# Performance work log

Measured on AMD Instinct MI355X. Metric: run time of the kernel, lower is better.

Reference implementation:

```python
import jax, jax.numpy as jnp
import numpy as np

B, S, D, L = 32, 1024, 768, 12

def setup_inputs() -> dict:
    key = jax.random.key(0)
    ks = jax.random.split(key, 10)
    hidden_states = jax.random.normal(ks[0], (B, S, D), dtype=jnp.float32)
    Wq = jax.random.normal(ks[1], (L, D, D), dtype=jnp.float32) * 0.02
    Wk = jax.random.normal(ks[2], (L, D, D), dtype=jnp.float32) * 0.02
    Wv = jax.random.normal(ks[3], (L, D, D), dtype=jnp.float32) * 0.02
    bq = jnp.zeros((L, D), dtype=jnp.float32)
    bk = jnp.zeros((L, D), dtype=jnp.float32)
    bv = jnp.zeros((L, D), dtype=jnp.float32)
    l_k = jnp.full((L, D), 0.8, dtype=jnp.float32)  # iA3 scales, init 0.8 per source
    l_v = jnp.full((L, D), 0.8, dtype=jnp.float32)
    W_head = jax.random.normal(ks[4], (D, 1), dtype=jnp.float32) * 0.02
    b_head = jnp.zeros((1,), dtype=jnp.float32)
    return {"hidden_states": hidden_states, "Wq": Wq, "bq": bq, "Wk": Wk, "bk": bk,
            "Wv": Wv, "bv": bv, "l_k": l_k, "l_v": l_v, "W_head": W_head, "b_head": b_head}

def reference(hidden_states, Wq, bq, Wk, bk, Wv, bv, l_k, l_v, W_head, b_head):
    scale = 1.0 / jnp.sqrt(jnp.float32(D))

    def layer_step(h, params):
        wq, bq_i, wk, bk_i, wv, bv_i, lk, lv = params
        Q = jnp.einsum('bsd,de->bse', h, wq) + bq_i
        K = (jnp.einsum('bsd,de->bse', h, wk) + bk_i) * lk  # iA3 per-channel scale on K
        V = (jnp.einsum('bsd,de->bse', h, wv) + bv_i) * lv  # iA3 per-channel scale on V
        attn = jax.nn.softmax(jnp.einsum('bqd,bkd->bqk', Q, K) * scale, axis=-1)
        h_new = jnp.einsum('bqk,bkd->bqd', attn, V)  # note: no residual/LN, matches source
        return h_new, None

    h, _ = jax.lax.scan(layer_step, hidden_states, (Wq, bq, Wk, bk, Wv, bv, l_k, l_v))
    pooled = h[:, 0, :]  # CLS token
    out = pooled @ W_head + b_head  # [B, 1]
    return out[:, 0]
```

## Files before the change

kernel.cpp:

```cpp
#include <hip/hip_runtime.h>
#include <hip/hip_fp16.h>
#include <math.h>

#define B_ 32
#define S_ 1024
#define D_ 768
#define L_ 12
#define SD 786432LL
#define SS 1048576LL
#define DD 589824LL
#define LDL 1769472LL

typedef _Float16 half8 __attribute__((ext_vector_type(8)));
typedef float f32x4 __attribute__((ext_vector_type(4)));
typedef unsigned short u16;

#define SW(lr) ((((lr) ^ ((lr) >> 3)) & 7))

#define GLD16(p, o) __builtin_amdgcn_global_load_lds( \
        (const __attribute__((address_space(1))) void*)(p), \
        (__attribute__((address_space(3))) void*)&smem[o], 16, 0, 0)


__global__ __launch_bounds__(256, 3)
void gemm_qkv_k(const __half* __restrict__ A, const __half* __restrict__ Wt,
                const float* __restrict__ biasC, const float* __restrict__ scaleC,
                float aBias,
                __half* __restrict__ CQ, __half* __restrict__ CK, __half* __restrict__ CVt,
                int nBase, int tilesX, int mPerXcd)
{
    __shared__ __align__(16) u16 smem[24576];
    const int K = 768;

    const int flat = blockIdx.x;
    const int xcd = flat & 7;
    const int jj = flat >> 3;
    const int mLocal = jj / tilesX;
    const int nxI = jj - mLocal * tilesX;
    const int n0 = nxI * 128;
    const int m0 = (xcd * mPerXcd + mLocal) * 128;

    const int t = threadIdx.x;
    const int l = t & 63, w = t >> 6;
    const int wm = (w & 1) * 64, wn = (w >> 1) * 64;

    const int u0 = t, u1 = t + 256;
    const int r0 = u0 >> 2, c0 = (u0 & 3) ^ ((r0 >> 1) & 3);
    const int r1 = u1 >> 2, c1 = (u1 & 3) ^ ((r1 >> 1) & 3);
    const __half* gA0 = A + (long long)(m0 + r0) * K + c0 * 8;
    const __half* gA1 = A + (long long)(m0 + r1) * K + c1 * 8;
    const __half* gB0 = Wt + (long long)(n0 + r0) * K + c0 * 8;
    const __half* gB1 = Wt + (long long)(n0 + r1) * K + c1 * 8;

    int aoff[4], boff[4];
    const int kc = l >> 4;
    #pragma unroll
    for (int mt = 0; mt < 4; ++mt) {
        int rr = wm + mt * 16 + (l & 15);
        aoff[mt] = (rr * 4 + (kc ^ ((rr >> 1) & 3))) * 8;
        int rb = wn + mt * 16 + (l & 15);
        boff[mt] = (rb * 4 + (kc ^ ((rb >> 1) & 3))) * 8;
    }

    f32x4 acc[4][4];
    #pragma unroll
    for (int i = 0; i < 4; ++i)
        #pragma unroll
        for (int j = 0; j < 4; ++j)
            acc[i][j] = (f32x4){0.f, 0.f, 0.f, 0.f};

    GLD16(gA0,      u0 * 8);                 GLD16(gA1,      u1 * 8);
    GLD16(gB0,      12288 + u0 * 8);         GLD16(gB1,      12288 + u1 * 8);
    GLD16(gA0 + 32, 4096 + u0 * 8);          GLD16(gA1 + 32, 4096 + u1 * 8);
    GLD16(gB0 + 32, 12288 + 4096 + u0 * 8);  GLD16(gB1 + 32, 12288 + 4096 + u1 * 8);

    int cur = 0;
    #pragma unroll 3
    for (int k0 = 0; k0 < K; k0 += 32) {
        if (k0 + 32 < K) asm volatile("s_waitcnt vmcnt(4)\n\ts_barrier" ::: "memory");
        else             asm volatile("s_waitcnt vmcnt(0)\n\ts_barrier" ::: "memory");
        if (k0 + 64 < K) {
            const int ts = (cur + 2 >= 3) ? (cur - 1) : (cur + 2);
            const int tsa = ts * 4096, tsb = 12288 + ts * 4096;
            GLD16(gA0 + k0 + 64, tsa + u0 * 8);  GLD16(gA1 + k0 + 64, tsa + u1 * 8);
            GLD16(gB0 + k0 + 64, tsb + u0 * 8);  GLD16(gB1 + k0 + 64, tsb + u1 * 8);
        }
        const int sa = cur * 4096, sb = 12288 + cur * 4096;
        half8 af[4], bf[4];
        #pragma unroll
        for (int mt = 0; mt < 4; ++mt) af[mt] = *(const half8*)(const void*)&smem[sa + aoff[mt]];
        #pragma unroll
        for (int nt = 0; nt < 4; ++nt) bf[nt] = *(const half8*)(const void*)&smem[sb + boff[nt]];
        #pragma unroll
        for (int nt = 0; nt < 4; ++nt)
            #pragma unroll
            for (int mt = 0; mt < 4; ++mt)
                acc[mt][nt] = __builtin_amdgcn_mfma_f32_16x16x32_f16(af[mt], bf[nt], acc[mt][nt], 0, 0, 0);
        __builtin_amdgcn_sched_barrier(0);
        cur = (cur >= 2) ? 0 : (cur + 1);
    }
    __syncthreads();

    const int nCat0 = n0 + nBase;
    const int region = nCat0 / 768;
    const int colBase = nCat0 - region * 768;

    float badd[4], bmul[4];
    #pragma unroll
    for (int nt = 0; nt < 4; ++nt) {
        int gn = nCat0 + wn + nt * 16 + (l & 15);
        badd[nt] = aBias * biasC[gn];
        bmul[nt] = scaleC[gn];
    }

    const int qbase = w * 4096;
    #pragma unroll
    for (int mt = 0; mt < 4; ++mt) {
        #pragma unroll
        for (int nt = 0; nt < 4; ++nt) {
            #pragma unroll
            for (int i = 0; i < 4; ++i) {
                int lrow = mt * 16 + ((l >> 4) << 2) + i;
                int lcol = nt * 16 + (l & 15);
                float v = (acc[mt][nt][i] + badd[nt]) * bmul[nt];
                int cc = lcol >> 3, c7 = lcol & 7;
                smem[qbase + lrow * 64 + ((cc ^ SW(lrow)) << 3) + c7] =
                    __half_as_ushort(__float2half(v));
            }
        }
    }
    __syncthreads();

    if (region < 2) {
        __half* Creg = region ? CK : CQ;
        #pragma unroll
        for (int p = 0; p < 8; ++p) {
            int u = t + p * 256;
            int R = u >> 4, cc = u & 15;
            int qb = ((R >> 6) + ((cc >> 3) << 1)) * 4096;
            int lr = R & 63, lcc = cc & 7;
            half8 val = *(const half8*)(const void*)&smem[qb + lr * 64 + ((lcc ^ SW(lr)) << 3)];
            *(half8*)(void*)&Creg[(long long)(m0 + R) * 768 + colBase + cc * 8] = val;
        }
    } else {
        #pragma unroll
        for (int p = 0; p < 8; ++p) {
            int u = t + p * 256;
            int Crow = u >> 4, mcc = u & 15;
            __align__(16) u16 tmp[8];
            #pragma unroll
            for (int j = 0; j < 8; ++j) {
                int m = mcc * 8 + j;
                int qb = ((m >> 6) + ((Crow >> 6) << 1)) * 4096;
                int lr = m & 63, lcol = Crow & 63;
                int lcc = lcol >> 3;
                tmp[j] = smem[qb + lr * 64 + ((lcc ^ SW(lr)) << 3) + (lcol & 7)];
            }
            long long b = m0 >> 10;
            __half* dst = CVt + b * SD + (long long)(colBase + Crow) * 1024 + (m0 & 1023) + mcc * 8;
            *(half8*)(void*)dst = *(const half8*)(const void*)tmp;
        }
    }
}

template<int SWIZ, int MODE>
__global__ __launch_bounds__(256, 3)
void gemm_att_k(const __half* __restrict__ A, const __half* __restrict__ B,
                float aAcc, __half* __restrict__ C, int K, int ldc,
                long long sA, long long sB, long long sC,
                int tilesX, int tilesPB, int bpx,
                float* __restrict__ rsp, const float* __restrict__ invsum)
{
    __shared__ __align__(16) u16 smem[24576];
    float* sums = (float*)(void*)&smem[16384];

    int nxI, ny;
    long long bz;
    if (SWIZ) {
        int flat = blockIdx.x;
        int xcd = flat & 7;
        int j = flat >> 3;
        int bLocal = j / tilesPB;
        int tt = j - bLocal * tilesPB;
        bz = (long long)(xcd * bpx + bLocal);
        ny = tt / tilesX;
        nxI = tt - ny * tilesX;
    } else {
        nxI = blockIdx.x; ny = blockIdx.y; bz = blockIdx.z;
    }

    const int t = threadIdx.x;
    const int l = t & 63, w = t >> 6;
    const int n0 = nxI * 128;
    const int m0 = ny * 128;
    A += bz * sA; B += bz * sB; C += bz * sC;

    const int wm = (w & 1) * 64, wn = (w >> 1) * 64;

    const int u0 = t, u1 = t + 256;
    const int r0 = u0 >> 2, c0 = (u0 & 3) ^ ((r0 >> 1) & 3);
    const int r1 = u1 >> 2, c1 = (u1 & 3) ^ ((r1 >> 1) & 3);
    const __half* gA0 = A + (long long)(m0 + r0) * K + c0 * 8;
    const __half* gA1 = A + (long long)(m0 + r1) * K + c1 * 8;
    const __half* gB0 = B + (long long)(n0 + r0) * K + c0 * 8;
    const __half* gB1 = B + (long long)(n0 + r1) * K + c1 * 8;

    int aoff[4], boff[4];
    const int kc = l >> 4;
    #pragma unroll
    for (int mt = 0; mt < 4; ++mt) {
        int rr = wm + mt * 16 + (l & 15);
        aoff[mt] = (rr * 4 + (kc ^ ((rr >> 1) & 3))) * 8;
        int rb = wn + mt * 16 + (l & 15);
        boff[mt] = (rb * 4 + (kc ^ ((rb >> 1) & 3))) * 8;
    }

    f32x4 acc[4][4];
    #pragma unroll
    for (int i = 0; i < 4; ++i)
        #pragma unroll
        for (int j = 0; j < 4; ++j)
            acc[i][j] = (f32x4){0.f, 0.f, 0.f, 0.f};

    GLD16(gA0,      u0 * 8);                 GLD16(gA1,      u1 * 8);
    GLD16(gB0,      12288 + u0 * 8);         GLD16(gB1,      12288 + u1 * 8);
    GLD16(gA0 + 32, 4096 + u0 * 8);          GLD16(gA1 + 32, 4096 + u1 * 8);
    GLD16(gB0 + 32, 12288 + 4096 + u0 * 8);  GLD16(gB1 + 32, 12288 + 4096 + u1 * 8);

    int cur = 0;
    #pragma unroll 3
    for (int k0 = 0; k0 < K; k0 += 32) {
        if (k0 + 32 < K) asm volatile("s_waitcnt vmcnt(4)\n\ts_barrier" ::: "memory");
        else             asm volatile("s_waitcnt vmcnt(0)\n\ts_barrier" ::: "memory");
        if (k0 + 64 < K) {
            const int ts = (cur + 2 >= 3) ? (cur - 1) : (cur + 2);
            const int tsa = ts * 4096, tsb = 12288 + ts * 4096;
            GLD16(gA0 + k0 + 64, tsa + u0 * 8);  GLD16(gA1 + k0 + 64, tsa + u1 * 8);
            GLD16(gB0 + k0 + 64, tsb + u0 * 8);  GLD16(gB1 + k0 + 64, tsb + u1 * 8);
        }
        const int sa = cur * 4096, sb = 12288 + cur * 4096;
        half8 af[4], bf[4];
        #pragma unroll
        for (int mt = 0; mt < 4; ++mt) af[mt] = *(const half8*)(const void*)&smem[sa + aoff[mt]];
        #pragma unroll
        for (int nt = 0; nt < 4; ++nt) bf[nt] = *(const half8*)(const void*)&smem[sb + boff[nt]];
        #pragma unroll
        for (int nt = 0; nt < 4; ++nt)
            #pragma unroll
            for (int mt = 0; mt < 4; ++mt)
                acc[mt][nt] = __builtin_amdgcn_mfma_f32_16x16x32_f16(af[mt], bf[nt], acc[mt][nt], 0, 0, 0);
        __builtin_amdgcn_sched_barrier(0);
        cur = (cur >= 2) ? 0 : (cur + 1);
    }
    __syncthreads();

    float invr[4][4];
    if (MODE == 2) {
        #pragma unroll
        for (int mt = 0; mt < 4; ++mt)
            #pragma unroll
            for (int i = 0; i < 4; ++i)
                invr[mt][i] = invsum[bz * 1024 + m0 + wm + mt * 16 + ((l >> 4) << 2) + i];
    }

    const int qbase = w * 4096;
    #pragma unroll
    for (int mt = 0; mt < 4; ++mt) {
        #pragma unroll
        for (int nt = 0; nt < 4; ++nt) {
            #pragma unroll
            for (int i = 0; i < 4; ++i) {
                int lrow = mt * 16 + ((l >> 4) << 2) + i;
                int lcol = nt * 16 + (l & 15);
                float v;
                if (MODE == 1)      v = __expf(acc[mt][nt][i] * aAcc);
                else                v = acc[mt][nt][i] * aAcc * invr[mt][i];
                int cc = lcol >> 3, c7 = lcol & 7;
                smem[qbase + lrow * 64 + ((cc ^ SW(lrow)) << 3) + c7] =
                    __half_as_ushort(__float2half(v));
            }
        }
    }
    __syncthreads();

    #pragma unroll
    for (int p = 0; p < 8; ++p) {
        int u = t + p * 256;
        int R = u >> 4, cc = u & 15;
        int qb = ((R >> 6) + ((cc >> 3) << 1)) * 4096;
        int lr = R & 63, lcc = cc & 7;
        half8 val = *(const half8*)(const void*)&smem[qb + lr * 64 + ((lcc ^ SW(lr)) << 3)];
        *(half8*)(void*)&C[(long long)(m0 + R) * ldc + n0 + cc * 8] = val;
        if (MODE == 1) {
            float s8 = 0.f;
            #pragma unroll
            for (int j = 0; j < 8; ++j) s8 += (float)val[j];
            sums[R * 17 + cc] = s8;
        }
    }
    if (MODE == 1) {
        __syncthreads();
        if (t < 128) {
            float s = 0.f;
            #pragma unroll
            for (int c = 0; c < 16; ++c) s += sums[t * 17 + c];
            rsp[bz * 8192 + (long long)(m0 + t) * 8 + nxI] = s;
        }
    }
}

__global__ __launch_bounds__(256)
void rowsuminv_k(const float* __restrict__ rsp, float* __restrict__ inv, int n)
{
    int i = blockIdx.x * 256 + threadIdx.x;
    if (i < n) {
        const float* p = rsp + (long long)i * 8;
        float s = ((p[0] + p[1]) + (p[2] + p[3])) + ((p[4] + p[5]) + (p[6] + p[7]));
        inv[i] = 1.0f / s;
    }
}

__global__ __launch_bounds__(256)
void cvt32to16_k(const float* __restrict__ X, __half* __restrict__ Y)
{
    long long i = ((long long)blockIdx.x * 256 + threadIdx.x) * 4;
    float4 v = *(const float4*)&X[i];
    *(__half2*)&Y[i]     = __floats2half2_rn(v.x, v.y);
    *(__half2*)&Y[i + 2] = __floats2half2_rn(v.z, v.w);
}

__global__ __launch_bounds__(256)
void wtrans_k(const float* __restrict__ W, __half* __restrict__ Wt,
              long long ldL, int rowOff)
{
    __shared__ float Ls[64][65];
    const int lyr = blockIdx.z;
    const int k0 = blockIdx.y * 64, n0 = blockIdx.x * 64;
    const float* src = W + (long long)lyr * DD;
    __half* dst = Wt + (long long)lyr * ldL;
    const int t = threadIdx.x;
    #pragma unroll
    for (int p = 0; p < 4; ++p) {
        int u = t + p * 256;
        int r = u >> 4, c4 = (u & 15) * 4;
        float4 v = *(const float4*)&src[(long long)(k0 + r) * D_ + n0 + c4];
        Ls[r][c4] = v.x; Ls[r][c4 + 1] = v.y; Ls[r][c4 + 2] = v.z; Ls[r][c4 + 3] = v.w;
    }
    __syncthreads();
    #pragma unroll
    for (int p = 0; p < 2; ++p) {
        int u = t + p * 256;
        int n = u >> 3, kc8 = (u & 7) * 8;
        __align__(16) u16 tmp[8];
        #pragma unroll
        for (int j = 0; j < 8; ++j) {
            _Float16 h = (_Float16)Ls[kc8 + j][n];
            tmp[j] = *(const u16*)&h;
        }
        *(half8*)(void*)&dst[(long long)(rowOff + n0 + n) * D_ + k0 + kc8] =
            *(const half8*)(const void*)tmp;
    }
}

__global__ __launch_bounds__(256)
void bscat_k(const float* __restrict__ bq, const float* __restrict__ bk,
             const float* __restrict__ bv, const float* __restrict__ lk,
             const float* __restrict__ lv, float* __restrict__ bsb,
             float* __restrict__ bss)
{
    int i = blockIdx.x * 256 + threadIdx.x;
    if (i >= L_ * 2304) return;
    int l = i / 2304, p = i - l * 2304;
    int r = p / 768, c = p - r * 768;
    float b, s;
    if (r == 0)      { b = bq[l * 768 + c]; s = 1.f; }
    else if (r == 1) { b = bk[l * 768 + c]; s = lk[l * 768 + c]; }
    else             { b = bv[l * 768 + c]; s = lv[l * 768 + c]; }
    bsb[i] = b; bss[i] = s;
}

__global__ __launch_bounds__(256)
void q0_k(const __half* __restrict__ H16, const __half* __restrict__ Wcat,
          const float* __restrict__ bq, float* __restrict__ q0f, float sig)
{
    const int b = blockIdx.x;
    const int n = blockIdx.y * 256 + threadIdx.x;
    const int t = threadIdx.x;
    __shared__ __half hrow[768];
    const __half* h = H16 + (long long)b * SD;
    hrow[t] = h[t]; hrow[t + 256] = h[t + 256]; hrow[t + 512] = h[t + 512];
    __syncthreads();
    const __half* wr = Wcat + 11LL * LDL + (long long)n * 768;
    float acc = 0.f;
    for (int k = 0; k < 768; ++k) acc += (float)hrow[k] * (float)wr[k];
    q0f[b * 768 + n] = acc + sig * bq[11 * 768 + n];
}

__global__ __launch_bounds__(256)
void s0_k(const float* __restrict__ q0f, const __half* __restrict__ K16,
          float* __restrict__ s0f, int b0, float aQK)
{
    const int z = blockIdx.x;
    const int b = b0 + z;
    const int s = blockIdx.y * 256 + threadIdx.x;
    const int t = threadIdx.x;
    __shared__ float qrow[768];
    qrow[t] = q0f[b * 768 + t];
    qrow[t + 256] = q0f[b * 768 + t + 256];
    qrow[t + 512] = q0f[b * 768 + t + 512];
    __syncthreads();
    const __half* kr = K16 + (long long)z * SD + (long long)s * 768;
    float acc = 0.f;
    for (int k = 0; k < 768; ++k) acc += qrow[k] * (float)kr[k];
    s0f[b * 1024 + s] = acc * aQK;
}

__global__ __launch_bounds__(256)
void sm0_k(float* __restrict__ s0f, int b0)
{
    float* p = s0f + (long long)(b0 + blockIdx.x) * 1024;
    const int t = threadIdx.x;
    float v[4];
    float mx = -1e30f;
    #pragma unroll
    for (int j = 0; j < 4; ++j) { v[j] = p[t + 256 * j]; mx = fmaxf(mx, v[j]); }
    __shared__ float red[256];
    red[t] = mx; __syncthreads();
    for (int s = 128; s > 0; s >>= 1) { if (t < s) red[t] = fmaxf(red[t], red[t + s]); __syncthreads(); }
    mx = red[0];
    __syncthreads();
    float sum = 0.f;
    #pragma unroll
    for (int j = 0; j < 4; ++j) { v[j] = __expf(v[j] - mx); sum += v[j]; }
    red[t] = sum; __syncthreads();
    for (int s = 128; s > 0; s >>= 1) { if (t < s) red[t] += red[t + s]; __syncthreads(); }
    const float inv = 1.0f / red[0];
    __syncthreads();
    #pragma unroll
    for (int j = 0; j < 4; ++j) p[t + 256 * j] = v[j] * inv;
}

__global__ __launch_bounds__(256)
void o0_k(const float* __restrict__ p0f, const __half* __restrict__ Vt16,
          float* __restrict__ o0f, int b0, float invSig)
{
    const int z = blockIdx.x;
    const int b = b0 + z;
    const int d = blockIdx.y * 256 + threadIdx.x;
    const int t = threadIdx.x;
    __shared__ float prow[1024];
    #pragma unroll
    for (int j = 0; j < 4; ++j) prow[t + 256 * j] = p0f[b * 1024 + t + 256 * j];
    __syncthreads();
    const __half* vr = Vt16 + (long long)z * SD + (long long)d * 1024;
    float acc = 0.f;
    for (int s = 0; s < 1024; ++s) acc += prow[s] * (float)vr[s];
    o0f[b * 768 + d] = acc * invSig;
}

__global__ __launch_bounds__(256)
void headf_k(const float* __restrict__ o0f, const float* __restrict__ Wh,
             const float* __restrict__ bh, float* __restrict__ out)
{
    const int b = blockIdx.x;
    const int t = threadIdx.x;
    float s = 0.f;
    for (int d = t; d < 768; d += 256) s += o0f[b * 768 + d] * Wh[d];
    __shared__ float red[256];
    red[t] = s; __syncthreads();
    for (int k = 128; k > 0; k >>= 1) { if (t < k) red[t] += red[t + k]; __syncthreads(); }
    if (t == 0) out[b] = red[0] + bh[0];
}

extern "C" void kernel_launch(void* const* d_in, const int* in_sizes, int n_in,
                              void* d_out, int out_size, void* d_ws, size_t ws_size,
                              hipStream_t stream)
{
    const float* hs = (const float*)d_in[0];
    const float* Wq = (const float*)d_in[1];
    const float* bq = (const float*)d_in[2];
    const float* Wk = (const float*)d_in[3];
    const float* bk = (const float*)d_in[4];
    const float* Wv = (const float*)d_in[5];
    const float* bv = (const float*)d_in[6];
    const float* lk = (const float*)d_in[7];
    const float* lv = (const float*)d_in[8];
    const float* Wh = (const float*)d_in[9];
    const float* bh = (const float*)d_in[10];
    float* outp = (float*)d_out;

    __half* H16  = (__half*)d_ws;
    __half* Wcat = H16 + (long long)B_ * SD;
    float*  bsb  = (float*)(Wcat + 12LL * LDL);
    float*  bss  = bsb + 12 * 2304;
    float*  q0f  = bss + 12 * 2304;
    float*  s0f  = q0f + 32 * 768;
    float*  o0f  = s0f + 32 * 1024;
    float*  rsp  = o0f + 32 * 768;
    float*  inv  = rsp + 32LL * 8192;
    __half* Q16  = (__half*)(inv + 32 * 1024);

    const size_t baseBytes = (size_t)((char*)Q16 - (char*)d_ws);
    const size_t perG = ((size_t)(3 * SD) + (size_t)SS) * 2;
    long long avail = (long long)ws_size - (long long)baseBytes;
    int G = (avail > 0) ? (int)(avail / perG) : 1;
    if (G >= 32) G = 32; else if (G >= 16) G = 16; else if (G >= 8) G = 8;
    if (G < 1) G = 1;
    __half* K16  = Q16 + (long long)G * SD;
    __half* Vt16 = K16 + (long long)G * SD;
    __half* P16  = Vt16 + (long long)G * SD;

    cvt32to16_k<<<dim3((int)((B_ * SD) / 1024)), 256, 0, stream>>>(hs, H16);
    wtrans_k<<<dim3(12, 12, 12), 256, 0, stream>>>(Wq, Wcat, LDL, 0);
    wtrans_k<<<dim3(12, 12, 12), 256, 0, stream>>>(Wk, Wcat, LDL, 768);
    wtrans_k<<<dim3(12, 12, 12), 256, 0, stream>>>(Wv, Wcat, LDL, 1536);
    bscat_k<<<dim3((L_ * 2304 + 255) / 256), 256, 0, stream>>>(bq, bk, bv, lk, lv, bsb, bss);

    const float scq = 0.036084391824351615f;
    float sig = 1.f;

    for (int lyr = 0; lyr < L_ - 1; ++lyr) {
        const __half* W = Wcat + (long long)lyr * LDL;
        const float* bb = bsb + lyr * 2304;
        const float* ss = bss + lyr * 2304;
        const float aQK = scq / (sig * sig);

        for (int b0 = 0; b0 < B_; b0 += G) {
            const int nb = (B_ - b0 < G) ? (B_ - b0) : G;
            const __half* hg = H16 + (long long)b0 * SD;

            gemm_qkv_k<<<dim3(18 * 8 * nb), 256, 0, stream>>>(
                hg, W, bb, ss, sig, Q16, K16, Vt16, 0, 18, nb);

            if ((nb & 7) == 0) {
                gemm_att_k<1, 1><<<dim3(nb * 64), 256, 0, stream>>>(
                    Q16, K16, aQK, P16, 768, 1024, SD, SD, SS, 8, 64, nb >> 3, rsp, nullptr);
            } else {
                gemm_att_k<0, 1><<<dim3(8, 8, nb), 256, 0, stream>>>(
                    Q16, K16, aQK, P16, 768, 1024, SD, SD, SS, 8, 64, 1, rsp, nullptr);
            }

            rowsuminv_k<<<dim3(nb * 4), 256, 0, stream>>>(rsp, inv, nb * 1024);

            if ((nb & 7) == 0) {
                gemm_att_k<1, 2><<<dim3(nb * 48), 256, 0, stream>>>(
                    P16, Vt16, 4.f, H16 + (long long)b0 * SD, 1024, 768, SS, SD, SD,
                    6, 48, nb >> 3, nullptr, inv);
            } else {
                gemm_att_k<0, 2><<<dim3(6, 8, nb), 256, 0, stream>>>(
                    P16, Vt16, 4.f, H16 + (long long)b0 * SD, 1024, 768, SS, SD, SD,
                    6, 48, 1, nullptr, inv);
            }
        }
        sig *= 4.f;
    }

    const float aQK = scq / (sig * sig);
    q0_k<<<dim3(B_, 3), 256, 0, stream>>>(H16, Wcat, bq, q0f, sig);

    for (int b0 = 0; b0 < B_; b0 += G) {
        const int nb = (B_ - b0 < G) ? (B_ - b0) : G;
        const __half* hg = H16 + (long long)b0 * SD;

        gemm_qkv_k<<<dim3(12 * 8 * nb), 256, 0, stream>>>(
            hg, Wcat + 11LL * LDL + 768LL * 768, bsb + 11 * 2304, bss + 11 * 2304,
            sig, K16 , K16, Vt16, 768, 12, nb);

        s0_k<<<dim3(nb, 4), 256, 0, stream>>>(q0f, K16, s0f, b0, aQK);
        sm0_k<<<dim3(nb), 256, 0, stream>>>(s0f, b0);
        o0_k<<<dim3(nb, 3), 256, 0, stream>>>(s0f, Vt16, o0f, b0, 1.f / sig);
    }

    headf_k<<<dim3(B_), 256, 0, stream>>>(o0f, Wh, bh, outp);
}
```

Measured before the change: 3.482 ms.

## Enlarge QKV and QK^T GEMM tiles to 256x128 with 8x4 MFMA per wave

The QKV projection and the QK^T score GEMM now use 256x128 output tiles: each wave computes 128x64 with 32 accumulators, and shared memory grows to 72KB with occupancy lowered to 2 blocks. The QK^T kernel is split from the PV kernel and computes row-sum partials with wave shuffles instead of a second LDS pass and barrier. The epilogue LDS layout becomes a single 128-column swizzled tile. Larger tiles raise arithmetic intensity per byte loaded, at the cost of fewer resident waves, higher register pressure and fewer blocks to fill the GPU.

```diff
diff --git a/kernel.cpp b/kernel.cpp
--- a/kernel.cpp
+++ b/kernel.cpp
@@ -22,80 +22,96 @@
         (__attribute__((address_space(3))) void*)&smem[o], 16, 0, 0)
 
 
-__global__ __launch_bounds__(256, 3)
+template<int SWIZ>
+__global__ __launch_bounds__(256, 2)
 void gemm_qkv_k(const __half* __restrict__ A, const __half* __restrict__ Wt,
                 const float* __restrict__ biasC, const float* __restrict__ scaleC,
                 float aBias,
                 __half* __restrict__ CQ, __half* __restrict__ CK, __half* __restrict__ CVt,
                 int nBase, int tilesX, int mPerXcd)
 {
-    __shared__ __align__(16) u16 smem[24576];
+    __shared__ __align__(16) u16 smem[36864];
     const int K = 768;
 
-    const int flat = blockIdx.x;
-    const int xcd = flat & 7;
-    const int jj = flat >> 3;
-    const int mLocal = jj / tilesX;
-    const int nxI = jj - mLocal * tilesX;
+    int mIdx, nxI;
+    if (SWIZ) {
+        const int flat = blockIdx.x;
+        const int xcd = flat & 7;
+        const int jj = flat >> 3;
+        const int mLocal = jj / tilesX;
+        nxI = jj - mLocal * tilesX;
+        mIdx = xcd * mPerXcd + mLocal;
+    } else {
+        mIdx = blockIdx.x / tilesX;
+        nxI = blockIdx.x - mIdx * tilesX;
+    }
+    const int m0 = mIdx * 256;
     const int n0 = nxI * 128;
-    const int m0 = (xcd * mPerXcd + mLocal) * 128;
 
     const int t = threadIdx.x;
     const int l = t & 63, w = t >> 6;
-    const int wm = (w & 1) * 64, wn = (w >> 1) * 64;
-
-    const int u0 = t, u1 = t + 256;
-    const int r0 = u0 >> 2, c0 = (u0 & 3) ^ ((r0 >> 1) & 3);
-    const int r1 = u1 >> 2, c1 = (u1 & 3) ^ ((r1 >> 1) & 3);
-    const __half* gA0 = A + (long long)(m0 + r0) * K + c0 * 8;
-    const __half* gA1 = A + (long long)(m0 + r1) * K + c1 * 8;
-    const __half* gB0 = Wt + (long long)(n0 + r0) * K + c0 * 8;
-    const __half* gB1 = Wt + (long long)(n0 + r1) * K + c1 * 8;
-
-    int aoff[4], boff[4];
-    const int kc = l >> 4;
-    #pragma unroll
-    for (int mt = 0; mt < 4; ++mt) {
-        int rr = wm + mt * 16 + (l & 15);
-        aoff[mt] = (rr * 4 + (kc ^ ((rr >> 1) & 3))) * 8;
-        int rb = wn + mt * 16 + (l & 15);
-        boff[mt] = (rb * 4 + (kc ^ ((rb >> 1) & 3))) * 8;
-    }
-
-    f32x4 acc[4][4];
-    #pragma unroll
-    for (int i = 0; i < 4; ++i)
+    const int wm = (w & 1) * 128, wn = (w >> 1) * 64;
+    const int q = l >> 4, lr = l & 15;
+
+    const int uA0 = t, uA1 = t + 256, uA2 = t + 512, uA3 = t + 768;
+    const int uB0 = t, uB1 = t + 256;
+#define MKA(u) (A + (long long)(m0 + ((u) >> 2)) * K + ((((u) & 3) ^ ((((u) >> 2) >> 1) & 3)) * 8))
+#define MKB(u) (Wt + (long long)(n0 + ((u) >> 2)) * K + ((((u) & 3) ^ ((((u) >> 2) >> 1) & 3)) * 8))
+    const __half* gA0 = MKA(uA0); const __half* gA1 = MKA(uA1);
+    const __half* gA2 = MKA(uA2); const __half* gA3 = MKA(uA3);
+    const __half* gB0 = MKB(uB0); const __half* gB1 = MKB(uB1);
+#undef MKA
+#undef MKB
+
+    int aoff[8], boff[4];
+    #pragma unroll
+    for (int mf = 0; mf < 8; ++mf) {
+        int rr = wm + mf * 16 + lr;
+        aoff[mf] = (rr * 4 + (q ^ ((rr >> 1) & 3))) * 8;
+    }
+    #pragma unroll
+    for (int nf = 0; nf < 4; ++nf) {
+        int rb = wn + nf * 16 + lr;
+        boff[nf] = (rb * 4 + (q ^ ((rb >> 1) & 3))) * 8;
+    }
+
+    f32x4 acc[8][4];
+    #pragma unroll
+    for (int i = 0; i < 8; ++i)
         #pragma unroll
         for (int j = 0; j < 4; ++j)
             acc[i][j] = (f32x4){0.f, 0.f, 0.f, 0.f};
 
-    GLD16(gA0,      u0 * 8);                 GLD16(gA1,      u1 * 8);
-    GLD16(gB0,      12288 + u0 * 8);         GLD16(gB1,      12288 + u1 * 8);
-    GLD16(gA0 + 32, 4096 + u0 * 8);          GLD16(gA1 + 32, 4096 + u1 * 8);
-    GLD16(gB0 + 32, 12288 + 4096 + u0 * 8);  GLD16(gB1 + 32, 12288 + 4096 + u1 * 8);
+    GLD16(gA0, uA0 * 8); GLD16(gA1, uA1 * 8); GLD16(gA2, uA2 * 8); GLD16(gA3, uA3 * 8);
+    GLD16(gB0, 8192 + uB0 * 8); GLD16(gB1, 8192 + uB1 * 8);
+    GLD16(gA0 + 32, 12288 + uA0 * 8); GLD16(gA1 + 32, 12288 + uA1 * 8);
+    GLD16(gA2 + 32, 12288 + uA2 * 8); GLD16(gA3 + 32, 12288 + uA3 * 8);
+    GLD16(gB0 + 32, 12288 + 8192 + uB0 * 8); GLD16(gB1 + 32, 12288 + 8192 + uB1 * 8);
 
     int cur = 0;
     #pragma unroll 3
     for (int k0 = 0; k0 < K; k0 += 32) {
-        if (k0 + 32 < K) asm volatile("s_waitcnt vmcnt(4)\n\ts_barrier" ::: "memory");
+        if (k0 + 32 < K) asm volatile("s_waitcnt vmcnt(6)\n\ts_barrier" ::: "memory");
         else             asm volatile("s_waitcnt vmcnt(0)\n\ts_barrier" ::: "memory");
         if (k0 + 64 < K) {
             const int ts = (cur + 2 >= 3) ? (cur - 1) : (cur + 2);
-            const int tsa = ts * 4096, tsb = 12288 + ts * 4096;
-            GLD16(gA0 + k0 + 64, tsa + u0 * 8);  GLD16(gA1 + k0 + 64, tsa + u1 * 8);
-            GLD16(gB0 + k0 + 64, tsb + u0 * 8);  GLD16(gB1 + k0 + 64, tsb + u1 * 8);
-        }
-        const int sa = cur * 4096, sb = 12288 + cur * 4096;
-        half8 af[4], bf[4];
-        #pragma unroll
-        for (int mt = 0; mt < 4; ++mt) af[mt] = *(const half8*)(const void*)&smem[sa + aoff[mt]];
-        #pragma unroll
-        for (int nt = 0; nt < 4; ++nt) bf[nt] = *(const half8*)(const void*)&smem[sb + boff[nt]];
-        #pragma unroll
-        for (int nt = 0; nt < 4; ++nt)
+            const int tb = ts * 12288;
+            GLD16(gA0 + k0 + 64, tb + uA0 * 8); GLD16(gA1 + k0 + 64, tb + uA1 * 8);
+            GLD16(gA2 + k0 + 64, tb + uA2 * 8); GLD16(gA3 + k0 + 64, tb + uA3 * 8);
+            GLD16(gB0 + k0 + 64, tb + 8192 + uB0 * 8);
+            GLD16(gB1 + k0 + 64, tb + 8192 + uB1 * 8);
+        }
+        const int sa = cur * 12288, sb = sa + 8192;
+        half8 af[8], bf[4];
+        #pragma unroll
+        for (int mf = 0; mf < 8; ++mf) af[mf] = *(const half8*)(const void*)&smem[sa + aoff[mf]];
+        #pragma unroll
+        for (int nf = 0; nf < 4; ++nf) bf[nf] = *(const half8*)(const void*)&smem[sb + boff[nf]];
+        #pragma unroll
+        for (int nf = 0; nf < 4; ++nf)
             #pragma unroll
-            for (int mt = 0; mt < 4; ++mt)
-                acc[mt][nt] = __builtin_amdgcn_mfma_f32_16x16x32_f16(af[mt], bf[nt], acc[mt][nt], 0, 0, 0);
+            for (int mf = 0; mf < 8; ++mf)
+                acc[mf][nf] = __builtin_amdgcn_mfma_f32_16x16x32_f16(af[mf], bf[nf], acc[mf][nf], 0, 0, 0);
         __builtin_amdgcn_sched_barrier(0);
         cur = (cur >= 2) ? 0 : (cur + 1);
     }
@@ -108,23 +124,22 @@
     float badd[4], bmul[4];
     #pragma unroll
     for (int nt = 0; nt < 4; ++nt) {
-        int gn = nCat0 + wn + nt * 16 + (l & 15);
+        int gn = nCat0 + wn + nt * 16 + lr;
         badd[nt] = aBias * biasC[gn];
         bmul[nt] = scaleC[gn];
     }
 
-    const int qbase = w * 4096;
-    #pragma unroll
-    for (int mt = 0; mt < 4; ++mt) {
+    #pragma unroll
+    for (int mf = 0; mf < 8; ++mf) {
         #pragma unroll
         for (int nt = 0; nt < 4; ++nt) {
             #pragma unroll
             for (int i = 0; i < 4; ++i) {
-                int lrow = mt * 16 + ((l >> 4) << 2) + i;
-                int lcol = nt * 16 + (l & 15);
-                float v = (acc[mt][nt][i] + badd[nt]) * bmul[nt];
+                int lrow = wm + mf * 16 + q * 4 + i;
+                int lcol = wn + nt * 16 + lr;
+                float v = (acc[mf][nt][i] + badd[nt]) * bmul[nt];
                 int cc = lcol >> 3, c7 = lcol & 7;
-                smem[qbase + lrow * 64 + ((cc ^ SW(lrow)) << 3) + c7] =
+                smem[lrow * 128 + ((cc ^ (lrow & 15)) << 3) + c7] =
                     __half_as_ushort(__float2half(v));
             }
         }
@@ -134,45 +149,39 @@
     if (region < 2) {
         __half* Creg = region ? CK : CQ;
         #pragma unroll
-        for (int p = 0; p < 8; ++p) {
+        for (int p = 0; p < 16; ++p) {
             int u = t + p * 256;
             int R = u >> 4, cc = u & 15;
-            int qb = ((R >> 6) + ((cc >> 3) << 1)) * 4096;
-            int lr = R & 63, lcc = cc & 7;
-            half8 val = *(const half8*)(const void*)&smem[qb + lr * 64 + ((lcc ^ SW(lr)) << 3)];
+            half8 val = *(const half8*)(const void*)&smem[R * 128 + ((cc ^ (R & 15)) << 3)];
             *(half8*)(void*)&Creg[(long long)(m0 + R) * 768 + colBase + cc * 8] = val;
         }
     } else {
-        #pragma unroll
-        for (int p = 0; p < 8; ++p) {
+        long long b = m0 >> 10;
+        const int mrow0 = m0 & 1023;
+        #pragma unroll
+        for (int p = 0; p < 16; ++p) {
             int u = t + p * 256;
-            int Crow = u >> 4, mcc = u & 15;
+            int n = u >> 5, mc = u & 31;
             __align__(16) u16 tmp[8];
             #pragma unroll
             for (int j = 0; j < 8; ++j) {
-                int m = mcc * 8 + j;
-                int qb = ((m >> 6) + ((Crow >> 6) << 1)) * 4096;
-                int lr = m & 63, lcol = Crow & 63;
-                int lcc = lcol >> 3;
-                tmp[j] = smem[qb + lr * 64 + ((lcc ^ SW(lr)) << 3) + (lcol & 7)];
+                int m = mc * 8 + j;
+                tmp[j] = smem[m * 128 + ((((n >> 3) ^ (m & 15))) << 3) + (n & 7)];
             }
-            long long b = m0 >> 10;
-            __half* dst = CVt + b * SD + (long long)(colBase + Crow) * 1024 + (m0 & 1023) + mcc * 8;
+            __half* dst = CVt + b * SD + (long long)(colBase + n) * 1024 + mrow0 + mc * 8;
             *(half8*)(void*)dst = *(const half8*)(const void*)tmp;
         }
     }
 }
 
-template<int SWIZ, int MODE>
-__global__ __launch_bounds__(256, 3)
-void gemm_att_k(const __half* __restrict__ A, const __half* __restrict__ B,
-                float aAcc, __half* __restrict__ C, int K, int ldc,
-                long long sA, long long sB, long long sC,
-                int tilesX, int tilesPB, int bpx,
-                float* __restrict__ rsp, const float* __restrict__ invsum)
-{
-    __shared__ __align__(16) u16 smem[24576];
-    float* sums = (float*)(void*)&smem[16384];
+template<int SWIZ>
+__global__ __launch_bounds__(256, 2)
+void gemm_qk_k(const __half* __restrict__ A, const __half* __restrict__ B,
+               float aAcc, __half* __restrict__ C, float* __restrict__ rsp,
+               int tilesX, int tilesPB, int bpx)
+{
+    __shared__ __align__(16) u16 smem[36864];
+    const int K = 768;
 
     int nxI, ny;
     long long bz;
@@ -191,6 +200,139 @@
 
     const int t = threadIdx.x;
     const int l = t & 63, w = t >> 6;
+    const int m0 = ny * 256;
+    const int n0 = nxI * 128;
+    A += bz * SD; B += bz * SD; C += bz * SS;
+
+    const int wm = (w & 1) * 128, wn = (w >> 1) * 64;
+    const int q = l >> 4, lr = l & 15;
+
+    const int uA0 = t, uA1 = t + 256, uA2 = t + 512, uA3 = t + 768;
+    const int uB0 = t, uB1 = t + 256;
+#define MKA(u) (A + (long long)(m0 + ((u) >> 2)) * K + ((((u) & 3) ^ ((((u) >> 2) >> 1) & 3)) * 8))
+#define MKB(u) (B + (long long)(n0 + ((u) >> 2)) * K + ((((u) & 3) ^ ((((u) >> 2) >> 1) & 3)) * 8))
+    const __half* gA0 = MKA(uA0); const __half* gA1 = MKA(uA1);
+    const __half* gA2 = MKA(uA2); const __half* gA3 = MKA(uA3);
+    const __half* gB0 = MKB(uB0); const __half* gB1 = MKB(uB1);
+#undef MKA
+#undef MKB
+
+    int aoff[8], boff[4];
+    #pragma unroll
+    for (int mf = 0; mf < 8; ++mf) {
+        int rr = wm + mf * 16 + lr;
+        aoff[mf] = (rr * 4 + (q ^ ((rr >> 1) & 3))) * 8;
+    }
+    #pragma unroll
+    for (int nf = 0; nf < 4; ++nf) {
+        int rb = wn + nf * 16 + lr;
+        boff[nf] = (rb * 4 + (q ^ ((rb >> 1) & 3))) * 8;
+    }
+
+    f32x4 acc[8][4];
+    #pragma unroll
+    for (int i = 0; i < 8; ++i)
+        #pragma unroll
+        for (int j = 0; j < 4; ++j)
+            acc[i][j] = (f32x4){0.f, 0.f, 0.f, 0.f};
+
+    GLD16(gA0, uA0 * 8); GLD16(gA1, uA1 * 8); GLD16(gA2, uA2 * 8); GLD16(gA3, uA3 * 8);
+    GLD16(gB0, 8192 + uB0 * 8); GLD16(gB1, 8192 + uB1 * 8);
+    GLD16(gA0 + 32, 12288 + uA0 * 8); GLD16(gA1 + 32, 12288 + uA1 * 8);
+    GLD16(gA2 + 32, 12288 + uA2 * 8); GLD16(gA3 + 32, 12288 + uA3 * 8);
+    GLD16(gB0 + 32, 12288 + 8192 + uB0 * 8); GLD16(gB1 + 32, 12288 + 8192 + uB1 * 8);
+
+    int cur = 0;
+    #pragma unroll 3
+    for (int k0 = 0; k0 < K; k0 += 32) {
+        if (k0 + 32 < K) asm volatile("s_waitcnt vmcnt(6)\n\ts_barrier" ::: "memory");
+        else             asm volatile("s_waitcnt vmcnt(0)\n\ts_barrier" ::: "memory");
+        if (k0 + 64 < K) {
+            const int ts = (cur + 2 >= 3) ? (cur - 1) : (cur + 2);
+            const int tb = ts * 12288;
+            GLD16(gA0 + k0 + 64, tb + uA0 * 8); GLD16(gA1 + k0 + 64, tb + uA1 * 8);
+            GLD16(gA2 + k0 + 64, tb + uA2 * 8); GLD16(gA3 + k0 + 64, tb + uA3 * 8);
+            GLD16(gB0 + k0 + 64, tb + 8192 + uB0 * 8);
+            GLD16(gB1 + k0 + 64, tb + 8192 + uB1 * 8);
+        }
+        const int sa = cur * 12288, sb = sa + 8192;
+        half8 af[8], bf[4];
+        #pragma unroll
+        for (int mf = 0; mf < 8; ++mf) af[mf] = *(const half8*)(const void*)&smem[sa + aoff[mf]];
+        #pragma unroll
+        for (int nf = 0; nf < 4; ++nf) bf[nf] = *(const half8*)(const void*)&smem[sb + boff[nf]];
+        #pragma unroll
+        for (int nf = 0; nf < 4; ++nf)
+            #pragma unroll
+            for (int mf = 0; mf < 8; ++mf)
+                acc[mf][nf] = __builtin_amdgcn_mfma_f32_16x16x32_f16(af[mf], bf[nf], acc[mf][nf], 0, 0, 0);
+        __builtin_amdgcn_sched_barrier(0);
+        cur = (cur >= 2) ? 0 : (cur + 1);
+    }
+    __syncthreads();
+
+    #pragma unroll
+    for (int mf = 0; mf < 8; ++mf) {
+        #pragma unroll
+        for (int nt = 0; nt < 4; ++nt) {
+            #pragma unroll
+            for (int i = 0; i < 4; ++i) {
+                int lrow = wm + mf * 16 + q * 4 + i;
+                int lcol = wn + nt * 16 + lr;
+                float v = __expf(acc[mf][nt][i] * aAcc);
+                int cc = lcol >> 3, c7 = lcol & 7;
+                smem[lrow * 128 + ((cc ^ (lrow & 15)) << 3) + c7] =
+                    __half_as_ushort(__float2half(v));
+            }
+        }
+    }
+    __syncthreads();
+
+    #pragma unroll
+    for (int p = 0; p < 16; ++p) {
+        int u = t + p * 256;
+        int R = u >> 4, cc = u & 15;
+        half8 val = *(const half8*)(const void*)&smem[R * 128 + ((cc ^ (R & 15)) << 3)];
+        *(half8*)(void*)&C[(long long)(m0 + R) * 1024 + n0 + cc * 8] = val;
+        float s8 = 0.f;
+        #pragma unroll
+        for (int j = 0; j < 8; ++j) s8 += (float)val[j];
+        s8 += __shfl_xor(s8, 1, 16);
+        s8 += __shfl_xor(s8, 2, 16);
+        s8 += __shfl_xor(s8, 4, 16);
+        s8 += __shfl_xor(s8, 8, 16);
+        if ((l & 15) == 0)
+            rsp[bz * 8192 + (long long)(m0 + R) * 8 + nxI] = s8;
+    }
+}
+
+template<int SWIZ>
+__global__ __launch_bounds__(256, 3)
+void gemm_pv_k(const __half* __restrict__ A, const __half* __restrict__ B,
+               float aAcc, __half* __restrict__ C, int K, int ldc,
+               long long sA, long long sB, long long sC,
+               int tilesX, int tilesPB, int bpx,
+               const float* __restrict__ invsum)
+{
+    __shared__ __align__(16) u16 smem[24576];
+
+    int nxI, ny;
+    long long bz;
+    if (SWIZ) {
+        int flat = blockIdx.x;
+        int xcd = flat & 7;
+        int j = flat >> 3;
+        int bLocal = j / tilesPB;
+        int tt = j - bLocal * tilesPB;
+        bz = (long long)(xcd * bpx + bLocal);
+        ny = tt / tilesX;
+        nxI = tt - ny * tilesX;
+    } else {
+        nxI = blockIdx.x; ny = blockIdx.y; bz = blockIdx.z;
+    }
+
+    const int t = threadIdx.x;
+    const int l = t & 63, w = t >> 6;
     const int n0 = nxI * 128;
     const int m0 = ny * 128;
     A += bz * sA; B += bz * sB; C += bz * sC;
@@ -255,13 +397,11 @@
     __syncthreads();
 
     float invr[4][4];
-    if (MODE == 2) {
-        #pragma unroll
-        for (int mt = 0; mt < 4; ++mt)
-            #pragma unroll
-            for (int i = 0; i < 4; ++i)
-                invr[mt][i] = invsum[bz * 1024 + m0 + wm + mt * 16 + ((l >> 4) << 2) + i];
-    }
+    #pragma unroll
+    for (int mt = 0; mt < 4; ++mt)
+        #pragma unroll
+        for (int i = 0; i < 4; ++i)
+            invr[mt][i] = invsum[bz * 1024 + m0 + wm + mt * 16 + ((l >> 4) << 2) + i];
 
     const int qbase = w * 4096;
     #pragma unroll
@@ -272,9 +412,7 @@
             for (int i = 0; i < 4; ++i) {
                 int lrow = mt * 16 + ((l >> 4) << 2) + i;
                 int lcol = nt * 16 + (l & 15);
-                float v;
-                if (MODE == 1)      v = __expf(acc[mt][nt][i] * aAcc);
-                else                v = acc[mt][nt][i] * aAcc * invr[mt][i];
+                float v = acc[mt][nt][i] * aAcc * invr[mt][i];
                 int cc = lcol >> 3, c7 = lcol & 7;
                 smem[qbase + lrow * 64 + ((cc ^ SW(lrow)) << 3) + c7] =
                     __half_as_ushort(__float2half(v));
@@ -288,24 +426,9 @@
         int u = t + p * 256;
         int R = u >> 4, cc = u & 15;
         int qb = ((R >> 6) + ((cc >> 3) << 1)) * 4096;
-        int lr = R & 63, lcc = cc & 7;
-        half8 val = *(const half8*)(const void*)&smem[qb + lr * 64 + ((lcc ^ SW(lr)) << 3)];
+        int lr2 = R & 63, lcc = cc & 7;
+        half8 val = *(const half8*)(const void*)&smem[qb + lr2 * 64 + ((lcc ^ SW(lr2)) << 3)];
         *(half8*)(void*)&C[(long long)(m0 + R) * ldc + n0 + cc * 8] = val;
-        if (MODE == 1) {
-            float s8 = 0.f;
-            #pragma unroll
-            for (int j = 0; j < 8; ++j) s8 += (float)val[j];
-            sums[R * 17 + cc] = s8;
-        }
-    }
-    if (MODE == 1) {
-        __syncthreads();
-        if (t < 128) {
-            float s = 0.f;
-            #pragma unroll
-            for (int c = 0; c < 16; ++c) s += sums[t * 17 + c];
-            rsp[bz * 8192 + (long long)(m0 + t) * 8 + nxI] = s;
-        }
     }
 }
 
@@ -529,27 +652,32 @@
             const int nb = (B_ - b0 < G) ? (B_ - b0) : G;
             const __half* hg = H16 + (long long)b0 * SD;
 
-            gemm_qkv_k<<<dim3(18 * 8 * nb), 256, 0, stream>>>(
-                hg, W, bb, ss, sig, Q16, K16, Vt16, 0, 18, nb);
+            if ((nb & 1) == 0) {
+                gemm_qkv_k<1><<<dim3(8 * (nb >> 1) * 18), 256, 0, stream>>>(
+                    hg, W, bb, ss, sig, Q16, K16, Vt16, 0, 18, nb >> 1);
+            } else {
+                gemm_qkv_k<0><<<dim3(nb * 4 * 18), 256, 0, stream>>>(
+                    hg, W, bb, ss, sig, Q16, K16, Vt16, 0, 18, 0);
+            }
 
             if ((nb & 7) == 0) {
-                gemm_att_k<1, 1><<<dim3(nb * 64), 256, 0, stream>>>(
-                    Q16, K16, aQK, P16, 768, 1024, SD, SD, SS, 8, 64, nb >> 3, rsp, nullptr);
+                gemm_qk_k<1><<<dim3(nb * 32), 256, 0, stream>>>(
+                    Q16, K16, aQK, P16, rsp, 8, 32, nb >> 3);
             } else {
-                gemm_att_k<0, 1><<<dim3(8, 8, nb), 256, 0, stream>>>(
-                    Q16, K16, aQK, P16, 768, 1024, SD, SD, SS, 8, 64, 1, rsp, nullptr);
+                gemm_qk_k<0><<<dim3(8, 4, nb), 256, 0, stream>>>(
+                    Q16, K16, aQK, P16, rsp, 8, 32, 1);
             }
 
             rowsuminv_k<<<dim3(nb * 4), 256, 0, stream>>>(rsp, inv, nb * 1024);
 
             if ((nb & 7) == 0) {
-                gemm_att_k<1, 2><<<dim3(nb * 48), 256, 0, stream>>>(
+                gemm_pv_k<1><<<dim3(nb * 48), 256, 0, stream>>>(
                     P16, Vt16, 4.f, H16 + (long long)b0 * SD, 1024, 768, SS, SD, SD,
-                    6, 48, nb >> 3, nullptr, inv);
+                    6, 48, nb >> 3, inv);
             } else {
-                gemm_att_k<0, 2><<<dim3(6, 8, nb), 256, 0, stream>>>(
+                gemm_pv_k<0><<<dim3(6, 8, nb), 256, 0, stream>>>(
                     P16, Vt16, 4.f, H16 + (long long)b0 * SD, 1024, 768, SS, SD, SD,
-                    6, 48, 1, nullptr, inv);
+                    6, 48, 1, inv);
             }
         }
         sig *= 4.f;
@@ -562,9 +690,15 @@
         const int nb = (B_ - b0 < G) ? (B_ - b0) : G;
         const __half* hg = H16 + (long long)b0 * SD;
 
-        gemm_qkv_k<<<dim3(12 * 8 * nb), 256, 0, stream>>>(
-            hg, Wcat + 11LL * LDL + 768LL * 768, bsb + 11 * 2304, bss + 11 * 2304,
-            sig, K16 , K16, Vt16, 768, 12, nb);
+        if ((nb & 1) == 0) {
+            gemm_qkv_k<1><<<dim3(8 * (nb >> 1) * 12), 256, 0, stream>>>(
+                hg, Wcat + 11LL * LDL + 768LL * 768, bsb + 11 * 2304, bss + 11 * 2304,
+                sig, K16 , K16, Vt16, 768, 12, nb >> 1);
+        } else {
+            gemm_qkv_k<0><<<dim3(nb * 4 * 12), 256, 0, stream>>>(
+                hg, Wcat + 11LL * LDL + 768LL * 768, bsb + 11 * 2304, bss + 11 * 2304,
+                sig, K16 , K16, Vt16, 768, 12, 0);
+        }
 
         s0_k<<<dim3(nb, 4), 256, 0, stream>>>(q0f, K16, s0f, b0, aQK);
         sm0_k<<<dim3(nb), 256, 0, stream>>>(s0f, b0);
```

Result: slower. 3.796 ms (+9.0%).

## Enlarge QKV GEMM tile to 256x128 with per-wave 128x64 sub-tiles

Applied to the files above, without the earlier changes.

The QKV projection GEMM now computes 256x128 output tiles instead of 128x128, with each wave holding a 128x64 accumulator block (8x4 MFMA fragments). This doubles A-side reuse of each B fragment and halves the number of blocks. Shared memory grows to 72 KB, launch bounds drop to 2 blocks per CU, and the epilogue is rewritten with a 128-wide swizzled staging layout. A non-XCD-swizzled variant covers odd batch-group counts. The cost is higher register pressure and fewer resident waves.

```diff
diff --git a/kernel.cpp b/kernel.cpp
--- a/kernel.cpp
+++ b/kernel.cpp
@@ -16,86 +16,102 @@
 typedef unsigned short u16;
 
 #define SW(lr) ((((lr) ^ ((lr) >> 3)) & 7))
+#define KEY16(r) (((r) ^ ((r) >> 3)) & 15)
 
 #define GLD16(p, o) __builtin_amdgcn_global_load_lds( \
         (const __attribute__((address_space(1))) void*)(p), \
         (__attribute__((address_space(3))) void*)&smem[o], 16, 0, 0)
 
-
-__global__ __launch_bounds__(256, 3)
+template<int SWIZ>
+__global__ __launch_bounds__(256, 2)
 void gemm_qkv_k(const __half* __restrict__ A, const __half* __restrict__ Wt,
                 const float* __restrict__ biasC, const float* __restrict__ scaleC,
                 float aBias,
                 __half* __restrict__ CQ, __half* __restrict__ CK, __half* __restrict__ CVt,
                 int nBase, int tilesX, int mPerXcd)
 {
-    __shared__ __align__(16) u16 smem[24576];
+    __shared__ __align__(16) u16 smem[36864];
     const int K = 768;
 
-    const int flat = blockIdx.x;
-    const int xcd = flat & 7;
-    const int jj = flat >> 3;
-    const int mLocal = jj / tilesX;
-    const int nxI = jj - mLocal * tilesX;
+    int mIdx, nxI;
+    if (SWIZ) {
+        const int flat = blockIdx.x;
+        const int xcd = flat & 7;
+        const int jj = flat >> 3;
+        const int mLocal = jj / tilesX;
+        nxI = jj - mLocal * tilesX;
+        mIdx = xcd * mPerXcd + mLocal;
+    } else {
+        mIdx = blockIdx.x / tilesX;
+        nxI = blockIdx.x - mIdx * tilesX;
+    }
+    const int m0 = mIdx * 256;
     const int n0 = nxI * 128;
-    const int m0 = (xcd * mPerXcd + mLocal) * 128;
 
     const int t = threadIdx.x;
     const int l = t & 63, w = t >> 6;
-    const int wm = (w & 1) * 64, wn = (w >> 1) * 64;
-
-    const int u0 = t, u1 = t + 256;
-    const int r0 = u0 >> 2, c0 = (u0 & 3) ^ ((r0 >> 1) & 3);
-    const int r1 = u1 >> 2, c1 = (u1 & 3) ^ ((r1 >> 1) & 3);
-    const __half* gA0 = A + (long long)(m0 + r0) * K + c0 * 8;
-    const __half* gA1 = A + (long long)(m0 + r1) * K + c1 * 8;
-    const __half* gB0 = Wt + (long long)(n0 + r0) * K + c0 * 8;
-    const __half* gB1 = Wt + (long long)(n0 + r1) * K + c1 * 8;
-
-    int aoff[4], boff[4];
-    const int kc = l >> 4;
-    #pragma unroll
-    for (int mt = 0; mt < 4; ++mt) {
-        int rr = wm + mt * 16 + (l & 15);
-        aoff[mt] = (rr * 4 + (kc ^ ((rr >> 1) & 3))) * 8;
-        int rb = wn + mt * 16 + (l & 15);
-        boff[mt] = (rb * 4 + (kc ^ ((rb >> 1) & 3))) * 8;
-    }
-
-    f32x4 acc[4][4];
-    #pragma unroll
-    for (int i = 0; i < 4; ++i)
+    const int wm = (w & 1) * 128, wn = (w >> 1) * 64;
+    const int q = l >> 4, lr = l & 15;
+
+    const int uA0 = t, uA1 = t + 256, uA2 = t + 512, uA3 = t + 768;
+    const int uB0 = t, uB1 = t + 256;
+#define MKA(u) (A + (long long)(m0 + ((u) >> 2)) * K + ((((u) & 3) ^ ((((u) >> 2) >> 1) & 3)) * 8))
+#define MKB(u) (Wt + (long long)(n0 + ((u) >> 2)) * K + ((((u) & 3) ^ ((((u) >> 2) >> 1) & 3)) * 8))
+    const __half* gA0 = MKA(uA0); const __half* gA1 = MKA(uA1);
+    const __half* gA2 = MKA(uA2); const __half* gA3 = MKA(uA3);
+    const __half* gB0 = MKB(uB0); const __half* gB1 = MKB(uB1);
+#undef MKA
+#undef MKB
+
+    int aoff[8], boff[4];
+    #pragma unroll
+    for (int mf = 0; mf < 8; ++mf) {
+        int rr = wm + mf * 16 + lr;
+        aoff[mf] = (rr * 4 + (q ^ ((rr >> 1) & 3))) * 8;
+    }
+    #pragma unroll
+    for (int nf = 0; nf < 4; ++nf) {
+        int rb = wn + nf * 16 + lr;
+        boff[nf] = (rb * 4 + (q ^ ((rb >> 1) & 3))) * 8;
+    }
+
+    f32x4 acc[8][4];
+    #pragma unroll
+    for (int i = 0; i < 8; ++i)
         #pragma unroll
         for (int j = 0; j < 4; ++j)
             acc[i][j] = (f32x4){0.f, 0.f, 0.f, 0.f};
 
-    GLD16(gA0,      u0 * 8);                 GLD16(gA1,      u1 * 8);
-    GLD16(gB0,      12288 + u0 * 8);         GLD16(gB1,      12288 + u1 * 8);
-    GLD16(gA0 + 32, 4096 + u0 * 8);          GLD16(gA1 + 32, 4096 + u1 * 8);
-    GLD16(gB0 + 32, 12288 + 4096 + u0 * 8);  GLD16(gB1 + 32, 12288 + 4096 + u1 * 8);
+    GLD16(gA0, uA0 * 8); GLD16(gA1, uA1 * 8); GLD16(gA2, uA2 * 8); GLD16(gA3, uA3 * 8);
+    GLD16(gB0, 8192 + uB0 * 8); GLD16(gB1, 8192 + uB1 * 8);
+    GLD16(gA0 + 32, 12288 + uA0 * 8); GLD16(gA1 + 32, 12288 + uA1 * 8);
+    GLD16(gA2 + 32, 12288 + uA2 * 8); GLD16(gA3 + 32, 12288 + uA3 * 8);
+    GLD16(gB0 + 32, 12288 + 8192 + uB0 * 8); GLD16(gB1 + 32, 12288 + 8192 + uB1 * 8);
 
     int cur = 0;
     #pragma unroll 3
     for (int k0 = 0; k0 < K; k0 += 32) {
-        if (k0 + 32 < K) asm volatile("s_waitcnt vmcnt(4)\n\ts_barrier" ::: "memory");
+        if (k0 + 32 < K) asm volatile("s_waitcnt vmcnt(6)\n\ts_barrier" ::: "memory");
         else             asm volatile("s_waitcnt vmcnt(0)\n\ts_barrier" ::: "memory");
         if (k0 + 64 < K) {
             const int ts = (cur + 2 >= 3) ? (cur - 1) : (cur + 2);
-            const int tsa = ts * 4096, tsb = 12288 + ts * 4096;
-            GLD16(gA0 + k0 + 64, tsa + u0 * 8);  GLD16(gA1 + k0 + 64, tsa + u1 * 8);
-            GLD16(gB0 + k0 + 64, tsb + u0 * 8);  GLD16(gB1 + k0 + 64, tsb + u1 * 8);
-        }
-        const int sa = cur * 4096, sb = 12288 + cur * 4096;
-        half8 af[4], bf[4];
-        #pragma unroll
-        for (int mt = 0; mt < 4; ++mt) af[mt] = *(const half8*)(const void*)&smem[sa + aoff[mt]];
-        #pragma unroll
-        for (int nt = 0; nt < 4; ++nt) bf[nt] = *(const half8*)(const void*)&smem[sb + boff[nt]];
-        #pragma unroll
-        for (int nt = 0; nt < 4; ++nt)
-            #pragma unroll
-            for (int mt = 0; mt < 4; ++mt)
-                acc[mt][nt] = __builtin_amdgcn_mfma_f32_16x16x32_f16(af[mt], bf[nt], acc[mt][nt], 0, 0, 0);
+            const int tb = ts * 12288;
+            GLD16(gA0 + k0 + 64, tb + uA0 * 8); GLD16(gA1 + k0 + 64, tb + uA1 * 8);
+            GLD16(gA2 + k0 + 64, tb + uA2 * 8); GLD16(gA3 + k0 + 64, tb + uA3 * 8);
+            GLD16(gB0 + k0 + 64, tb + 8192 + uB0 * 8);
+            GLD16(gB1 + k0 + 64, tb + 8192 + uB1 * 8);
+        }
+        const int sa = cur * 12288, sb = sa + 8192;
+        half8 af[8], bf[4];
+        #pragma unroll
+        for (int mf = 0; mf < 8; ++mf) af[mf] = *(const half8*)(const void*)&smem[sa + aoff[mf]];
+        #pragma unroll
+        for (int nf = 0; nf < 4; ++nf) bf[nf] = *(const half8*)(const void*)&smem[sb + boff[nf]];
+        #pragma unroll
+        for (int nf = 0; nf < 4; ++nf)
+            #pragma unroll
+            for (int mf = 0; mf < 8; ++mf)
+                acc[mf][nf] = __builtin_amdgcn_mfma_f32_16x16x32_f16(af[mf], bf[nf], acc[mf][nf], 0, 0, 0);
         __builtin_amdgcn_sched_barrier(0);
         cur = (cur >= 2) ? 0 : (cur + 1);
     }
@@ -108,23 +124,22 @@
     float badd[4], bmul[4];
     #pragma unroll
     for (int nt = 0; nt < 4; ++nt) {
-        int gn = nCat0 + wn + nt * 16 + (l & 15);
+        int gn = nCat0 + wn + nt * 16 + lr;
         badd[nt] = aBias * biasC[gn];
         bmul[nt] = scaleC[gn];
     }
 
-    const int qbase = w * 4096;
-    #pragma unroll
-    for (int mt = 0; mt < 4; ++mt) {
+    #pragma unroll
+    for (int mf = 0; mf < 8; ++mf) {
         #pragma unroll
         for (int nt = 0; nt < 4; ++nt) {
             #pragma unroll
             for (int i = 0; i < 4; ++i) {
-                int lrow = mt * 16 + ((l >> 4) << 2) + i;
-                int lcol = nt * 16 + (l & 15);
-                float v = (acc[mt][nt][i] + badd[nt]) * bmul[nt];
+                int lrow = wm + mf * 16 + q * 4 + i;
+                int lcol = wn + nt * 16 + lr;
+                float v = (acc[mf][nt][i] + badd[nt]) * bmul[nt];
                 int cc = lcol >> 3, c7 = lcol & 7;
-                smem[qbase + lrow * 64 + ((cc ^ SW(lrow)) << 3) + c7] =
+                smem[lrow * 128 + ((cc ^ KEY16(lrow)) << 3) + c7] =
                     __half_as_ushort(__float2half(v));
             }
         }
@@ -134,30 +149,26 @@
     if (region < 2) {
         __half* Creg = region ? CK : CQ;
         #pragma unroll
-        for (int p = 0; p < 8; ++p) {
+        for (int p = 0; p < 16; ++p) {
             int u = t + p * 256;
             int R = u >> 4, cc = u & 15;
-            int qb = ((R >> 6) + ((cc >> 3) << 1)) * 4096;
-            int lr = R & 63, lcc = cc & 7;
-            half8 val = *(const half8*)(const void*)&smem[qb + lr * 64 + ((lcc ^ SW(lr)) << 3)];
+            half8 val = *(const half8*)(const void*)&smem[R * 128 + ((cc ^ KEY16(R)) << 3)];
             *(half8*)(void*)&Creg[(long long)(m0 + R) * 768 + colBase + cc * 8] = val;
         }
     } else {
-        #pragma unroll
-        for (int p = 0; p < 8; ++p) {
+        long long b = m0 >> 10;
+        const int mrow0 = m0 & 1023;
+        #pragma unroll
+        for (int p = 0; p < 16; ++p) {
             int u = t + p * 256;
-            int Crow = u >> 4, mcc = u & 15;
+            int n = u >> 5, mc = u & 31;
             __align__(16) u16 tmp[8];
             #pragma unroll
             for (int j = 0; j < 8; ++j) {
-                int m = mcc * 8 + j;
-                int qb = ((m >> 6) + ((Crow >> 6) << 1)) * 4096;
-                int lr = m & 63, lcol = Crow & 63;
-                int lcc = lcol >> 3;
-                tmp[j] = smem[qb + lr * 64 + ((lcc ^ SW(lr)) << 3) + (lcol & 7)];
+                int m = mc * 8 + j;
+                tmp[j] = smem[m * 128 + ((((n >> 3) ^ KEY16(m))) << 3) + (n & 7)];
             }
-            long long b = m0 >> 10;
-            __half* dst = CVt + b * SD + (long long)(colBase + Crow) * 1024 + (m0 & 1023) + mcc * 8;
+            __half* dst = CVt + b * SD + (long long)(colBase + n) * 1024 + mrow0 + mc * 8;
             *(half8*)(void*)dst = *(const half8*)(const void*)tmp;
         }
     }
@@ -529,8 +540,13 @@
             const int nb = (B_ - b0 < G) ? (B_ - b0) : G;
             const __half* hg = H16 + (long long)b0 * SD;
 
-            gemm_qkv_k<<<dim3(18 * 8 * nb), 256, 0, stream>>>(
-                hg, W, bb, ss, sig, Q16, K16, Vt16, 0, 18, nb);
+            if ((nb & 1) == 0) {
+                gemm_qkv_k<1><<<dim3(8 * (nb >> 1) * 18), 256, 0, stream>>>(
+                    hg, W, bb, ss, sig, Q16, K16, Vt16, 0, 18, nb >> 1);
+            } else {
+                gemm_qkv_k<0><<<dim3(nb * 4 * 18), 256, 0, stream>>>(
+                    hg, W, bb, ss, sig, Q16, K16, Vt16, 0, 18, 0);
+            }
 
             if ((nb & 7) == 0) {
                 gemm_att_k<1, 1><<<dim3(nb * 64), 256, 0, stream>>>(
@@ -562,9 +578,15 @@
         const int nb = (B_ - b0 < G) ? (B_ - b0) : G;
         const __half* hg = H16 + (long long)b0 * SD;
 
-        gemm_qkv_k<<<dim3(12 * 8 * nb), 256, 0, stream>>>(
-            hg, Wcat + 11LL * LDL + 768LL * 768, bsb + 11 * 2304, bss + 11 * 2304,
-            sig, K16 , K16, Vt16, 768, 12, nb);
+        if ((nb & 1) == 0) {
+            gemm_qkv_k<1><<<dim3(8 * (nb >> 1) * 12), 256, 0, stream>>>(
+                hg, Wcat + 11LL * LDL + 768LL * 768, bsb + 11 * 2304, bss + 11 * 2304,
+                sig, K16 , K16, Vt16, 768, 12, nb >> 1);
+        } else {
+            gemm_qkv_k<0><<<dim3(nb * 4 * 12), 256, 0, stream>>>(
+                hg, Wcat + 11LL * LDL + 768LL * 768, bsb + 11 * 2304, bss + 11 * 2304,
+                sig, K16 , K16, Vt16, 768, 12, 0);
+        }
 
         s0_k<<<dim3(nb, 4), 256, 0, stream>>>(q0f, K16, s0f, b0, aQK);
         sm0_k<<<dim3(nb), 256, 0, stream>>>(s0f, b0);
```

Measured after the change: 3.224 ms, median of 2. -7.4%, faster.
